# Optimization experiments

Hardware: AMD Instinct MI355X
Metric: run time of the kernel (lower is better)

The kernel has to match this reference:

```python
import jax, jax.numpy as jnp
import numpy as np

NL, B, L, D, V = 8, 8, 2048, 768, 50288
HALT_ID = 50277
EPS = 1e-5


def setup_inputs() -> dict:
    key = jax.random.key(0)
    ks = jax.random.split(key, 6)
    x_steps = jax.random.normal(ks[0], (NL, B, L, D), jnp.float32)
    residual_steps = jax.random.normal(ks[1], (NL, B, L, D), jnp.float32)
    norm_weight = jnp.ones((D,), jnp.float32)
    lm_head_weight = jax.random.normal(ks[2], (V, D), jnp.float32) * 0.02
    ans_starts = jax.random.randint(ks[3], (B,), 1, L)            # valid answer positions
    chain_lens = jax.random.randint(ks[4], (B,), 1, NL + 1)       # ragged chain lengths
    chain_targets = jax.random.randint(ks[5], (B, NL), 0, V)
    # last target of each chain is <HALT> (as in training data)
    chain_targets = chain_targets.at[jnp.arange(B), chain_lens - 1].set(HALT_ID)
    return {
        "x_steps": x_steps,
        "residual_steps": residual_steps,
        "norm_weight": norm_weight,
        "lm_head_weight": lm_head_weight,
        "ans_starts": ans_starts,
        "chain_targets": chain_targets,
        "chain_lens": chain_lens,
    }


def _forward(x_steps, residual_steps, norm_weight, lm_head_weight,
             ans_starts, chain_targets, chain_lens):
    n_loops, Bn, Ln, Dn = x_steps.shape
    Vn = lm_head_weight.shape[0]
    b_idx = jnp.arange(Bn)

    # gather the single answer position per batch (logits_step[b, as_-1, :])
    pos = jnp.clip(ans_starts - 1, 0, Ln - 1)                     # [B]
    xg = x_steps[:, b_idx, pos]                                   # [NL,B,D]
    rg = residual_steps[:, b_idx, pos]                            # [NL,B,D]

    # norm_f(x, residual, prenorm=False) == RMSNorm(x + residual)
    h = xg + rg
    h = h * jax.lax.rsqrt(jnp.mean(h * h, axis=-1, keepdims=True) + EPS) * norm_weight

    # lm_head on the gathered positions only (same math as full logits + gather)
    logits = jnp.einsum("lbd,vd->lbv", h, lm_head_weight)         # [NL,B,V]

    # target id: btgt[min(loop_i, len(btgt)-1)]
    loop_i = jnp.arange(n_loops)[:, None]                         # [NL,1]
    tidx = jnp.minimum(loop_i, chain_lens[None, :] - 1)           # [NL,B]
    tgt = chain_targets[b_idx[None, :], tidx]                     # [NL,B]

    valid = (ans_starts[None, :] >= 1) & (ans_starts[None, :] < Ln) & (tgt < Vn)
    vf = valid.astype(jnp.float32)

    # full-vocab cross entropy per (loop, batch)
    logZ = jax.scipy.special.logsumexp(logits, axis=-1)           # [NL,B]
    tgt_logit = jnp.take_along_axis(logits, tgt[..., None], axis=-1)[..., 0]
    ce = logZ - tgt_logit                                         # [NL,B]

    pred = jnp.argmax(logits, axis=-1)                            # [NL,B]
    correct = (pred == tgt).astype(jnp.float32)

    cnt = vf.sum(axis=1)                                          # valid per loop
    has = cnt > 0
    hasf = has.astype(jnp.float32)
    denom = jnp.maximum(cnt, 1.0)
    loop_loss = jnp.where(has, (ce * vf).sum(axis=1) / denom, 0.0)
    loop_acc = jnp.where(has, (correct * vf).sum(axis=1) / denom, 0.0)

    n_has = hasf.sum()
    avg_loss = (loop_loss * hasf).sum() / jnp.maximum(n_has, 1.0)
    avg_acc = (loop_acc * hasf).sum() / jnp.maximum(n_has, 1.0)

    # answer_acc = mean of step_accs[:-1] (drop last valid loop) if >1 valid loop
    last_valid = n_loops - 1 - jnp.argmax(has[::-1])
    drop_last = hasf * (jnp.arange(n_loops) != last_valid).astype(jnp.float32)
    ans_mask = jnp.where(n_has > 1, drop_last, hasf)
    answer_acc = jnp.where(ans_mask.sum() > 0,
                           (loop_acc * ans_mask).sum() / jnp.maximum(ans_mask.sum(), 1.0),
                           avg_acc)

    hm = vf * (tgt == HALT_ID).astype(jnp.float32)
    halt_acc = jnp.where(hm.sum() > 0,
                         (correct * hm).sum() / jnp.maximum(hm.sum(), 1.0),
                         0.0)
    return avg_loss, avg_acc, answer_acc, halt_acc


def reference(x_steps, residual_steps, norm_weight, lm_head_weight,
              ans_starts, chain_targets, chain_lens):
    return _forward(x_steps, residual_steps, norm_weight, lm_head_weight,
                    ans_starts, chain_targets, chain_lens)
```

## Files before the change

### kernel.cpp

```cpp
#include <hip/hip_runtime.h>
#include <hip/hip_bf16.h>
#include <math.h>

#define NLOOP 8
#define BB 8
#define LLEN 2048
#define DD 768
#define VV 50288
#define HALT 50277
#define EPSF 1e-5f

#define BN 64
#define BKK 32
#define KSTEPS (DD / BKK)
#define NBLK ((VV + BN - 1) / BN)
#define PFD 6

typedef short bf16x8 __attribute__((ext_vector_type(8)));
typedef float f32x4 __attribute__((ext_vector_type(4)));

#define LGKM_BARRIER() asm volatile("s_waitcnt lgkmcnt(0)\n\ts_barrier" ::: "memory")

__device__ __forceinline__ unsigned short f32_to_bf16(float f) {
    unsigned u = __builtin_bit_cast(unsigned, f);
    unsigned r = (u + 0x7FFFu + ((u >> 16) & 1u)) >> 16;
    return (unsigned short)r;
}

__global__ __launch_bounds__(256) void k_prep(
    const float* __restrict__ x, const float* __restrict__ res,
    const float* __restrict__ nw, const float* __restrict__ W,
    const int* __restrict__ ans_starts, const int* __restrict__ chain_targets,
    const int* __restrict__ chain_lens,
    unsigned short* __restrict__ hbf, float* __restrict__ tgt_logit,
    unsigned int* __restrict__ counter)
{
    if (blockIdx.x == 0 && threadIdx.x == 0) *counter = 0u;

    int lb = blockIdx.x, l = lb >> 3, b = lb & 7;
    int tid = threadIdx.x, lane = tid & 63, wave = tid >> 6;
    int as = ans_starts[b];
    int pos = as - 1;
    pos = pos < 0 ? 0 : (pos > LLEN - 1 ? LLEN - 1 : pos);
    size_t base = ((size_t)lb * LLEN + (size_t)pos) * DD;

    float hv[3];
    float ss = 0.f;
#pragma unroll
    for (int i = 0; i < 3; ++i) {
        int d = tid + i * 256;
        float v = x[base + d] + res[base + d];
        hv[i] = v;
        ss += v * v;
    }
#pragma unroll
    for (int off = 32; off; off >>= 1) ss += __shfl_down(ss, off);
    __shared__ float red[4];
    __shared__ float bc;
    if (lane == 0) red[wave] = ss;
    __syncthreads();
    if (tid == 0) bc = red[0] + red[1] + red[2] + red[3];
    __syncthreads();
    float rs = rsqrtf(bc / (float)DD + EPSF);

    int cl = chain_lens[b];
    int tix = l < cl - 1 ? l : cl - 1;
    int tgt = chain_targets[b * NLOOP + tix];
    bool tok = (tgt >= 0) && (tgt < VV);

    float dp = 0.f;
#pragma unroll
    for (int i = 0; i < 3; ++i) {
        int d = tid + i * 256;
        float h = hv[i] * rs * nw[d];
        hbf[(size_t)lb * DD + d] = f32_to_bf16(h);
        if (tok) dp += h * W[(size_t)tgt * DD + d];
    }
#pragma unroll
    for (int off = 32; off; off >>= 1) dp += __shfl_down(dp, off);
    __syncthreads();
    if (lane == 0) red[wave] = dp;
    __syncthreads();
    if (tid == 0) tgt_logit[lb] = red[0] + red[1] + red[2] + red[3];
}

__global__ __launch_bounds__(256, 2) void k_logits(
    const float* __restrict__ W, const unsigned short* __restrict__ hbf,
    float* __restrict__ pmax, float* __restrict__ psum, int* __restrict__ parg)
{
    __shared__ unsigned short Bs[2][64 * 56];

    int blk = blockIdx.x;
    int v0 = blk * BN;
    int tid = threadIdx.x;
    int wave = tid >> 6, lane = tid & 63, q = lane >> 4, c = lane & 15;

    const unsigned short* Ap = hbf + (size_t)(16 * wave + c) * DD + q * 8;
    bf16x8 A[KSTEPS];
#pragma unroll
    for (int ks = 0; ks < KSTEPS; ++ks)
        A[ks] = *(const bf16x8*)(Ap + ks * BKK);

    int r1 = tid >> 3, koff = (tid & 7) * 4;
    int vB0 = v0 + r1, vB1 = v0 + r1 + 32;
    const float* gB0 = W + (size_t)(vB0 < VV ? vB0 : 0) * DD + koff;
    const float* gB1 = W + (size_t)(vB1 < VV ? vB1 : 0) * DD + koff;

    f32x4 acc[4];
#pragma unroll
    for (int n = 0; n < 4; ++n) acc[n] = (f32x4){0.f, 0.f, 0.f, 0.f};

    auto stage_write = [&](int bufi, const f32x4& ra, const f32x4& rb) {
        ushort4 w0, w1;
        w0.x = f32_to_bf16(ra[0]); w0.y = f32_to_bf16(ra[1]);
        w0.z = f32_to_bf16(ra[2]); w0.w = f32_to_bf16(ra[3]);
        w1.x = f32_to_bf16(rb[0]); w1.y = f32_to_bf16(rb[1]);
        w1.z = f32_to_bf16(rb[2]); w1.w = f32_to_bf16(rb[3]);
        *(ushort4*)&Bs[bufi][r1 * 56 + koff] = w0;
        *(ushort4*)&Bs[bufi][(r1 + 32) * 56 + koff] = w1;
    };
    auto mfma_step = [&](int bufi, int ks) {
        bf16x8 f0 = *(const bf16x8*)&Bs[bufi][(c +  0) * 56 + q * 8];
        bf16x8 f1 = *(const bf16x8*)&Bs[bufi][(c + 16) * 56 + q * 8];
        bf16x8 f2 = *(const bf16x8*)&Bs[bufi][(c + 32) * 56 + q * 8];
        bf16x8 f3 = *(const bf16x8*)&Bs[bufi][(c + 48) * 56 + q * 8];
        acc[0] = __builtin_amdgcn_mfma_f32_16x16x32_bf16(A[ks], f0, acc[0], 0, 0, 0);
        acc[1] = __builtin_amdgcn_mfma_f32_16x16x32_bf16(A[ks], f1, acc[1], 0, 0, 0);
        acc[2] = __builtin_amdgcn_mfma_f32_16x16x32_bf16(A[ks], f2, acc[2], 0, 0, 0);
        acc[3] = __builtin_amdgcn_mfma_f32_16x16x32_bf16(A[ks], f3, acc[3], 0, 0, 0);
    };

    f32x4 pa[PFD], pb[PFD];
#pragma unroll
    for (int i = 0; i < PFD; ++i) {
        pa[i] = __builtin_nontemporal_load((const f32x4*)(gB0 + i * BKK));
        pb[i] = __builtin_nontemporal_load((const f32x4*)(gB1 + i * BKK));
    }

#pragma unroll
    for (int ks = 0; ks < KSTEPS; ++ks) {
        const int slot = ks % PFD;
        const int bufi = ks & 1;
        stage_write(bufi, pa[slot], pb[slot]);
        LGKM_BARRIER();
        if (ks + PFD < KSTEPS) {
            pa[slot] = __builtin_nontemporal_load((const f32x4*)(gB0 + (ks + PFD) * BKK));
            pb[slot] = __builtin_nontemporal_load((const f32x4*)(gB1 + (ks + PFD) * BKK));
        }
        mfma_step(bufi, ks);
    }

    const float NEGINF = -__builtin_inff();
#pragma unroll
    for (int r = 0; r < 4; ++r) {
        float val = NEGINF; int idx = 0x7fffffff;
#pragma unroll
        for (int n = 0; n < 4; ++n) {
            int colg = v0 + 16 * n + c;
            float v = (colg < VV) ? acc[n][r] : NEGINF;
            if (v > val || (v == val && colg < idx)) { val = v; idx = colg; }
        }
#pragma unroll
        for (int off = 1; off < 16; off <<= 1) {
            float ov = __shfl_xor(val, off);
            int oi = __shfl_xor(idx, off);
            if (ov > val || (ov == val && oi < idx)) { val = ov; idx = oi; }
        }
        float M = val;
        float e = 0.f;
#pragma unroll
        for (int n = 0; n < 4; ++n) {
            int colg = v0 + 16 * n + c;
            e += (colg < VV) ? __expf(acc[n][r] - M) : 0.f;
        }
#pragma unroll
        for (int off = 1; off < 16; off <<= 1) e += __shfl_xor(e, off);
        if (c == 0) {
            int row = 16 * wave + 4 * q + r;
            pmax[(size_t)row * NBLK + blk] = M;
            psum[(size_t)row * NBLK + blk] = e;
            parg[(size_t)row * NBLK + blk] = idx;
        }
    }
}

__global__ __launch_bounds__(256) void k_combine(
    const float* __restrict__ pmax, const float* __restrict__ psum,
    const int* __restrict__ parg, const float* __restrict__ tgt_logit,
    const int* __restrict__ ans_starts, const int* __restrict__ chain_targets,
    const int* __restrict__ chain_lens,
    float* __restrict__ logZ, int* __restrict__ pred,
    unsigned int* __restrict__ counter, float* __restrict__ out)
{
    int r = blockIdx.x;
    int tid = threadIdx.x;
    int wave = tid >> 6, lane = tid & 63;
    const float NEGINF = -__builtin_inff();

    const float* pm = pmax + (size_t)r * NBLK;
    const float* ps = psum + (size_t)r * NBLK;
    const int*   pa = parg + (size_t)r * NBLK;

    float M = NEGINF; int A_ = 0x7fffffff;
    for (int i = tid; i < NBLK; i += 256) {
        float m = pm[i];
        int a = pa[i];
        if (m > M || (m == M && a < A_)) { M = m; A_ = a; }
    }
#pragma unroll
    for (int off = 1; off < 64; off <<= 1) {
        float ov = __shfl_xor(M, off);
        int oa = __shfl_xor(A_, off);
        if (ov > M || (ov == M && oa < A_)) { M = ov; A_ = oa; }
    }
    __shared__ float sm[4]; __shared__ int sa[4]; __shared__ float ssum[4];
    __shared__ int lastflag;
    if (lane == 0) { sm[wave] = M; sa[wave] = A_; }
    __syncthreads();
    if (tid == 0) {
#pragma unroll
        for (int w = 1; w < 4; ++w)
            if (sm[w] > sm[0] || (sm[w] == sm[0] && sa[w] < sa[0])) { sm[0] = sm[w]; sa[0] = sa[w]; }
    }
    __syncthreads();
    float Mg = sm[0];

    float S = 0.f;
    for (int i = tid; i < NBLK; i += 256)
        S += ps[i] * __expf(pm[i] - Mg);
#pragma unroll
    for (int off = 1; off < 64; off <<= 1) S += __shfl_xor(S, off);
    if (lane == 0) ssum[wave] = S;
    __syncthreads();
    if (tid == 0) {
        float lz = Mg + logf(ssum[0] + ssum[1] + ssum[2] + ssum[3]);
        __hip_atomic_store(&logZ[r], lz, __ATOMIC_RELAXED, __HIP_MEMORY_SCOPE_AGENT);
        __hip_atomic_store(&pred[r], sa[0], __ATOMIC_RELAXED, __HIP_MEMORY_SCOPE_AGENT);
        __threadfence();
        unsigned int old = atomicAdd(counter, 1u);
        lastflag = (old == 63u) ? 1 : 0;
    }
    __syncthreads();
    if (lastflag == 0) return;

    __threadfence();
    __shared__ float lzs[64]; __shared__ int prs[64];
    if (tid < 64) {
        lzs[tid] = __hip_atomic_load(&logZ[tid], __ATOMIC_RELAXED, __HIP_MEMORY_SCOPE_AGENT);
        prs[tid] = __hip_atomic_load(&pred[tid], __ATOMIC_RELAXED, __HIP_MEMORY_SCOPE_AGENT);
    }
    __syncthreads();
    if (tid == 0) {
        float loop_loss[NLOOP], loop_acc[NLOOP], hasf[NLOOP];
        float n_has = 0.f, hms = 0.f, hcs = 0.f;
        for (int l = 0; l < NLOOP; ++l) {
            float cnt = 0.f, se = 0.f, sc = 0.f;
            for (int b = 0; b < BB; ++b) {
                int cl = chain_lens[b];
                int ti = l < cl - 1 ? l : cl - 1;
                int tgt = chain_targets[b * NLOOP + ti];
                int as = ans_starts[b];
                bool valid = (as >= 1) && (as < LLEN) && (tgt < VV);
                int idx = l * BB + b;
                float ce = lzs[idx] - tgt_logit[idx];
                float corr = (prs[idx] == tgt) ? 1.f : 0.f;
                if (valid) {
                    cnt += 1.f; se += ce; sc += corr;
                    if (tgt == HALT) { hms += 1.f; hcs += corr; }
                }
            }
            bool has = cnt > 0.f;
            hasf[l] = has ? 1.f : 0.f;
            n_has += hasf[l];
            float denom = cnt > 1.f ? cnt : 1.f;
            loop_loss[l] = has ? se / denom : 0.f;
            loop_acc[l]  = has ? sc / denom : 0.f;
        }
        float nn = n_has > 1.f ? n_has : 1.f;
        float avg_loss = 0.f, avg_acc = 0.f;
        for (int l = 0; l < NLOOP; ++l) {
            avg_loss += loop_loss[l] * hasf[l];
            avg_acc  += loop_acc[l]  * hasf[l];
        }
        avg_loss /= nn; avg_acc /= nn;
        int last_valid = NLOOP - 1;
        for (int l = NLOOP - 1; l >= 0; --l) if (hasf[l] > 0.f) { last_valid = l; break; }
        float ams = 0.f, aacc = 0.f;
        for (int l = 0; l < NLOOP; ++l) {
            float mask = (n_has > 1.f) ? (hasf[l] * ((l != last_valid) ? 1.f : 0.f)) : hasf[l];
            ams += mask; aacc += loop_acc[l] * mask;
        }
        float answer_acc = (ams > 0.f) ? (aacc / (ams > 1.f ? ams : 1.f)) : avg_acc;
        float halt_acc = (hms > 0.f) ? (hcs / (hms > 1.f ? hms : 1.f)) : 0.f;
        out[0] = avg_loss; out[1] = avg_acc; out[2] = answer_acc; out[3] = halt_acc;
    }
}

extern "C" void kernel_launch(void* const* d_in, const int* in_sizes, int n_in,
                              void* d_out, int out_size, void* d_ws, size_t ws_size,
                              hipStream_t stream) {
    const float* x   = (const float*)d_in[0];
    const float* res = (const float*)d_in[1];
    const float* nw  = (const float*)d_in[2];
    const float* W   = (const float*)d_in[3];
    const int* ans   = (const int*)d_in[4];
    const int* ct    = (const int*)d_in[5];
    const int* cl    = (const int*)d_in[6];
    float* out = (float*)d_out;

    char* ws = (char*)d_ws;
    unsigned short* hbf = (unsigned short*)ws;
    float* tgtl = (float*)(ws + 98304);
    size_t off = 98560;
    float* pmax = (float*)(ws + off);  off += (size_t)64 * NBLK * 4;
    float* psum = (float*)(ws + off);  off += (size_t)64 * NBLK * 4;
    int*   parg = (int*)  (ws + off);  off += (size_t)64 * NBLK * 4;
    float* logZ = (float*)(ws + off);  off += 256;
    int*   pred = (int*)  (ws + off);  off += 256;
    unsigned int* counter = (unsigned int*)(ws + off); off += 256;

    k_prep<<<64, 256, 0, stream>>>(x, res, nw, W, ans, ct, cl, hbf, tgtl, counter);
    k_logits<<<NBLK, 256, 0, stream>>>(W, hbf, pmax, psum, parg);
    k_combine<<<64, 256, 0, stream>>>(pmax, psum, parg, tgtl, ans, ct, cl,
                                      logZ, pred, counter, out);
}
```

Before: 59.82 us.

## Fuse prep, logits and combine into one persistent kernel with atomic grid sync

Merges the three kernels into one launch. The first 64 blocks compute the RMSNorm rows while every block prefetches its W tile, and all blocks spin on an atomic counter until the normalized rows are ready. The last 64 blocks to finish then do the per-row softmax combine, and the final block computes the metrics. The vocabulary tile grows from 64 to 128 rows with a shallower prefetch, and the non-temporal loads become plain loads. This removes launch gaps and lets the W stream start before the norm is done. It relies on all 393 blocks being co-resident, which the spin-waits need to avoid deadlock.

```diff
diff --git a/kernel.cpp b/kernel.cpp
--- a/kernel.cpp
+++ b/kernel.cpp
@@ -10,11 +10,11 @@
 #define HALT 50277
 #define EPSF 1e-5f
 
-#define BN 64
+#define BN2 128
 #define BKK 32
 #define KSTEPS (DD / BKK)
-#define NBLK ((VV + BN - 1) / BN)
-#define PFD 6
+#define NBLK2 ((VV + BN2 - 1) / BN2)
+#define PFD 4
 
 typedef short bf16x8 __attribute__((ext_vector_type(8)));
 typedef float f32x4 __attribute__((ext_vector_type(4)));
@@ -27,73 +27,96 @@
     return (unsigned short)r;
 }
 
-__global__ __launch_bounds__(256) void k_prep(
+__global__ __launch_bounds__(256, 2) void k_fused(
     const float* __restrict__ x, const float* __restrict__ res,
     const float* __restrict__ nw, const float* __restrict__ W,
     const int* __restrict__ ans_starts, const int* __restrict__ chain_targets,
     const int* __restrict__ chain_lens,
-    unsigned short* __restrict__ hbf, float* __restrict__ tgt_logit,
-    unsigned int* __restrict__ counter)
+    unsigned short* __restrict__ hbf, float* __restrict__ tgtl,
+    float* __restrict__ pmax, float* __restrict__ psum, int* __restrict__ parg,
+    float* __restrict__ logZ, int* __restrict__ pred,
+    unsigned int* __restrict__ counters, float* __restrict__ out)
 {
-    if (blockIdx.x == 0 && threadIdx.x == 0) *counter = 0u;
-
-    int lb = blockIdx.x, l = lb >> 3, b = lb & 7;
-    int tid = threadIdx.x, lane = tid & 63, wave = tid >> 6;
-    int as = ans_starts[b];
-    int pos = as - 1;
-    pos = pos < 0 ? 0 : (pos > LLEN - 1 ? LLEN - 1 : pos);
-    size_t base = ((size_t)lb * LLEN + (size_t)pos) * DD;
-
-    float hv[3];
-    float ss = 0.f;
-#pragma unroll
-    for (int i = 0; i < 3; ++i) {
-        int d = tid + i * 256;
-        float v = x[base + d] + res[base + d];
-        hv[i] = v;
-        ss += v * v;
-    }
-#pragma unroll
-    for (int off = 32; off; off >>= 1) ss += __shfl_down(ss, off);
-    __shared__ float red[4];
-    __shared__ float bc;
-    if (lane == 0) red[wave] = ss;
-    __syncthreads();
-    if (tid == 0) bc = red[0] + red[1] + red[2] + red[3];
-    __syncthreads();
-    float rs = rsqrtf(bc / (float)DD + EPSF);
-
-    int cl = chain_lens[b];
-    int tix = l < cl - 1 ? l : cl - 1;
-    int tgt = chain_targets[b * NLOOP + tix];
-    bool tok = (tgt >= 0) && (tgt < VV);
-
-    float dp = 0.f;
-#pragma unroll
-    for (int i = 0; i < 3; ++i) {
-        int d = tid + i * 256;
-        float h = hv[i] * rs * nw[d];
-        hbf[(size_t)lb * DD + d] = f32_to_bf16(h);
-        if (tok) dp += h * W[(size_t)tgt * DD + d];
-    }
-#pragma unroll
-    for (int off = 32; off; off >>= 1) dp += __shfl_down(dp, off);
-    __syncthreads();
-    if (lane == 0) red[wave] = dp;
-    __syncthreads();
-    if (tid == 0) tgt_logit[lb] = red[0] + red[1] + red[2] + red[3];
-}
-
-__global__ __launch_bounds__(256, 2) void k_logits(
-    const float* __restrict__ W, const unsigned short* __restrict__ hbf,
-    float* __restrict__ pmax, float* __restrict__ psum, int* __restrict__ parg)
-{
-    __shared__ unsigned short Bs[2][64 * 56];
-
-    int blk = blockIdx.x;
-    int v0 = blk * BN;
+    __shared__ unsigned short Bs[2][BN2 * 56];
+
+    int bid = blockIdx.x;
     int tid = threadIdx.x;
     int wave = tid >> 6, lane = tid & 63, q = lane >> 4, c = lane & 15;
+    int v0 = bid * BN2;
+
+    int r1 = tid >> 3, koff = (tid & 7) * 4;
+    int vB0 = v0 + r1, vB1 = v0 + r1 + 32, vB2 = v0 + r1 + 64, vB3 = v0 + r1 + 96;
+    const float* gB0 = W + (size_t)(vB0 < VV ? vB0 : 0) * DD + koff;
+    const float* gB1 = W + (size_t)(vB1 < VV ? vB1 : 0) * DD + koff;
+    const float* gB2 = W + (size_t)(vB2 < VV ? vB2 : 0) * DD + koff;
+    const float* gB3 = W + (size_t)(vB3 < VV ? vB3 : 0) * DD + koff;
+
+    f32x4 pf0[PFD], pf1[PFD], pf2[PFD], pf3[PFD];
+#pragma unroll
+    for (int i = 0; i < PFD; ++i) {
+        pf0[i] = *(const f32x4*)(gB0 + i * BKK);
+        pf1[i] = *(const f32x4*)(gB1 + i * BKK);
+        pf2[i] = *(const f32x4*)(gB2 + i * BKK);
+        pf3[i] = *(const f32x4*)(gB3 + i * BKK);
+    }
+
+    if (bid < 64) {
+        int b = bid & 7, l = bid >> 3;
+        int as = ans_starts[b];
+        int pos = as - 1;
+        pos = pos < 0 ? 0 : (pos > LLEN - 1 ? LLEN - 1 : pos);
+        size_t base = ((size_t)bid * LLEN + (size_t)pos) * DD;
+
+        float hv[3];
+        float ss = 0.f;
+#pragma unroll
+        for (int i = 0; i < 3; ++i) {
+            int d = tid + i * 256;
+            float v = x[base + d] + res[base + d];
+            hv[i] = v;
+            ss += v * v;
+        }
+#pragma unroll
+        for (int off = 32; off; off >>= 1) ss += __shfl_down(ss, off);
+        __shared__ float red[4];
+        __shared__ float bc;
+        if (lane == 0) red[wave] = ss;
+        __syncthreads();
+        if (tid == 0) bc = red[0] + red[1] + red[2] + red[3];
+        __syncthreads();
+        float rs = rsqrtf(bc / (float)DD + EPSF);
+
+        int cl = chain_lens[b];
+        int tix = l < cl - 1 ? l : cl - 1;
+        int tgt = chain_targets[b * NLOOP + tix];
+        bool tok = (tgt >= 0) && (tgt < VV);
+
+        float dp = 0.f;
+#pragma unroll
+        for (int i = 0; i < 3; ++i) {
+            int d = tid + i * 256;
+            float h = hv[i] * rs * nw[d];
+            hbf[(size_t)bid * DD + d] = f32_to_bf16(h);
+            if (tok) dp += h * W[(size_t)tgt * DD + d];
+        }
+#pragma unroll
+        for (int off = 32; off; off >>= 1) dp += __shfl_down(dp, off);
+        __syncthreads();
+        if (lane == 0) red[wave] = dp;
+        __syncthreads();
+        if (tid == 0) tgtl[bid] = red[0] + red[1] + red[2] + red[3];
+
+        __threadfence();
+        __syncthreads();
+        if (tid == 0) atomicAdd(&counters[0], 1u);
+    }
+
+    if (tid == 0) {
+        while (__hip_atomic_load(&counters[0], __ATOMIC_ACQUIRE, __HIP_MEMORY_SCOPE_AGENT) < 64u)
+            __builtin_amdgcn_s_sleep(8);
+    }
+    __syncthreads();
+    __threadfence();
 
     const unsigned short* Ap = hbf + (size_t)(16 * wave + c) * DD + q * 8;
     bf16x8 A[KSTEPS];
@@ -101,53 +124,37 @@
     for (int ks = 0; ks < KSTEPS; ++ks)
         A[ks] = *(const bf16x8*)(Ap + ks * BKK);
 
-    int r1 = tid >> 3, koff = (tid & 7) * 4;
-    int vB0 = v0 + r1, vB1 = v0 + r1 + 32;
-    const float* gB0 = W + (size_t)(vB0 < VV ? vB0 : 0) * DD + koff;
-    const float* gB1 = W + (size_t)(vB1 < VV ? vB1 : 0) * DD + koff;
-
-    f32x4 acc[4];
-#pragma unroll
-    for (int n = 0; n < 4; ++n) acc[n] = (f32x4){0.f, 0.f, 0.f, 0.f};
-
-    auto stage_write = [&](int bufi, const f32x4& ra, const f32x4& rb) {
-        ushort4 w0, w1;
-        w0.x = f32_to_bf16(ra[0]); w0.y = f32_to_bf16(ra[1]);
-        w0.z = f32_to_bf16(ra[2]); w0.w = f32_to_bf16(ra[3]);
-        w1.x = f32_to_bf16(rb[0]); w1.y = f32_to_bf16(rb[1]);
-        w1.z = f32_to_bf16(rb[2]); w1.w = f32_to_bf16(rb[3]);
-        *(ushort4*)&Bs[bufi][r1 * 56 + koff] = w0;
-        *(ushort4*)&Bs[bufi][(r1 + 32) * 56 + koff] = w1;
+    f32x4 acc[8];
+#pragma unroll
+    for (int n = 0; n < 8; ++n) acc[n] = (f32x4){0.f, 0.f, 0.f, 0.f};
+
+    auto st_row = [&](int bufi, int row, const f32x4& v) {
+        ushort4 w0;
+        w0.x = f32_to_bf16(v[0]); w0.y = f32_to_bf16(v[1]);
+        w0.z = f32_to_bf16(v[2]); w0.w = f32_to_bf16(v[3]);
+        *(ushort4*)&Bs[bufi][row * 56 + koff] = w0;
     };
-    auto mfma_step = [&](int bufi, int ks) {
-        bf16x8 f0 = *(const bf16x8*)&Bs[bufi][(c +  0) * 56 + q * 8];
-        bf16x8 f1 = *(const bf16x8*)&Bs[bufi][(c + 16) * 56 + q * 8];
-        bf16x8 f2 = *(const bf16x8*)&Bs[bufi][(c + 32) * 56 + q * 8];
-        bf16x8 f3 = *(const bf16x8*)&Bs[bufi][(c + 48) * 56 + q * 8];
-        acc[0] = __builtin_amdgcn_mfma_f32_16x16x32_bf16(A[ks], f0, acc[0], 0, 0, 0);
-        acc[1] = __builtin_amdgcn_mfma_f32_16x16x32_bf16(A[ks], f1, acc[1], 0, 0, 0);
-        acc[2] = __builtin_amdgcn_mfma_f32_16x16x32_bf16(A[ks], f2, acc[2], 0, 0, 0);
-        acc[3] = __builtin_amdgcn_mfma_f32_16x16x32_bf16(A[ks], f3, acc[3], 0, 0, 0);
-    };
-
-    f32x4 pa[PFD], pb[PFD];
-#pragma unroll
-    for (int i = 0; i < PFD; ++i) {
-        pa[i] = __builtin_nontemporal_load((const f32x4*)(gB0 + i * BKK));
-        pb[i] = __builtin_nontemporal_load((const f32x4*)(gB1 + i * BKK));
-    }
 
 #pragma unroll
     for (int ks = 0; ks < KSTEPS; ++ks) {
         const int slot = ks % PFD;
         const int bufi = ks & 1;
-        stage_write(bufi, pa[slot], pb[slot]);
+        st_row(bufi, r1,      pf0[slot]);
+        st_row(bufi, r1 + 32, pf1[slot]);
+        st_row(bufi, r1 + 64, pf2[slot]);
+        st_row(bufi, r1 + 96, pf3[slot]);
         LGKM_BARRIER();
         if (ks + PFD < KSTEPS) {
-            pa[slot] = __builtin_nontemporal_load((const f32x4*)(gB0 + (ks + PFD) * BKK));
-            pb[slot] = __builtin_nontemporal_load((const f32x4*)(gB1 + (ks + PFD) * BKK));
-        }
-        mfma_step(bufi, ks);
+            pf0[slot] = *(const f32x4*)(gB0 + (ks + PFD) * BKK);
+            pf1[slot] = *(const f32x4*)(gB1 + (ks + PFD) * BKK);
+            pf2[slot] = *(const f32x4*)(gB2 + (ks + PFD) * BKK);
+            pf3[slot] = *(const f32x4*)(gB3 + (ks + PFD) * BKK);
+        }
+#pragma unroll
+        for (int n = 0; n < 8; ++n) {
+            bf16x8 f = *(const bf16x8*)&Bs[bufi][(c + 16 * n) * 56 + q * 8];
+            acc[n] = __builtin_amdgcn_mfma_f32_16x16x32_bf16(A[ks], f, acc[n], 0, 0, 0);
+        }
     }
 
     const float NEGINF = -__builtin_inff();
@@ -155,7 +162,7 @@
     for (int r = 0; r < 4; ++r) {
         float val = NEGINF; int idx = 0x7fffffff;
 #pragma unroll
-        for (int n = 0; n < 4; ++n) {
+        for (int n = 0; n < 8; ++n) {
             int colg = v0 + 16 * n + c;
             float v = (colg < VV) ? acc[n][r] : NEGINF;
             if (v > val || (v == val && colg < idx)) { val = v; idx = colg; }
@@ -169,7 +176,7 @@
         float M = val;
         float e = 0.f;
 #pragma unroll
-        for (int n = 0; n < 4; ++n) {
+        for (int n = 0; n < 8; ++n) {
             int colg = v0 + 16 * n + c;
             e += (colg < VV) ? __expf(acc[n][r] - M) : 0.f;
         }
@@ -177,122 +184,125 @@
         for (int off = 1; off < 16; off <<= 1) e += __shfl_xor(e, off);
         if (c == 0) {
             int row = 16 * wave + 4 * q + r;
-            pmax[(size_t)row * NBLK + blk] = M;
-            psum[(size_t)row * NBLK + blk] = e;
-            parg[(size_t)row * NBLK + blk] = idx;
-        }
-    }
-}
-
-__global__ __launch_bounds__(256) void k_combine(
-    const float* __restrict__ pmax, const float* __restrict__ psum,
-    const int* __restrict__ parg, const float* __restrict__ tgt_logit,
-    const int* __restrict__ ans_starts, const int* __restrict__ chain_targets,
-    const int* __restrict__ chain_lens,
-    float* __restrict__ logZ, int* __restrict__ pred,
-    unsigned int* __restrict__ counter, float* __restrict__ out)
-{
-    int r = blockIdx.x;
-    int tid = threadIdx.x;
-    int wave = tid >> 6, lane = tid & 63;
-    const float NEGINF = -__builtin_inff();
-
-    const float* pm = pmax + (size_t)r * NBLK;
-    const float* ps = psum + (size_t)r * NBLK;
-    const int*   pa = parg + (size_t)r * NBLK;
-
-    float M = NEGINF; int A_ = 0x7fffffff;
-    for (int i = tid; i < NBLK; i += 256) {
-        float m = pm[i];
-        int a = pa[i];
-        if (m > M || (m == M && a < A_)) { M = m; A_ = a; }
-    }
-#pragma unroll
-    for (int off = 1; off < 64; off <<= 1) {
-        float ov = __shfl_xor(M, off);
-        int oa = __shfl_xor(A_, off);
-        if (ov > M || (ov == M && oa < A_)) { M = ov; A_ = oa; }
-    }
-    __shared__ float sm[4]; __shared__ int sa[4]; __shared__ float ssum[4];
-    __shared__ int lastflag;
-    if (lane == 0) { sm[wave] = M; sa[wave] = A_; }
+            pmax[(size_t)row * NBLK2 + bid] = M;
+            psum[(size_t)row * NBLK2 + bid] = e;
+            parg[(size_t)row * NBLK2 + bid] = idx;
+        }
+    }
+
+    __threadfence();
     __syncthreads();
+    __shared__ unsigned int s_old;
+    if (tid == 0) s_old = atomicAdd(&counters[1], 1u);
+    __syncthreads();
+    int crow = (int)s_old - (NBLK2 - 64);
+    if (crow < 0) return;
+
     if (tid == 0) {
-#pragma unroll
-        for (int w = 1; w < 4; ++w)
-            if (sm[w] > sm[0] || (sm[w] == sm[0] && sa[w] < sa[0])) { sm[0] = sm[w]; sa[0] = sa[w]; }
+        while (__hip_atomic_load(&counters[1], __ATOMIC_ACQUIRE, __HIP_MEMORY_SCOPE_AGENT) < (unsigned)NBLK2)
+            __builtin_amdgcn_s_sleep(8);
     }
     __syncthreads();
-    float Mg = sm[0];
-
-    float S = 0.f;
-    for (int i = tid; i < NBLK; i += 256)
-        S += ps[i] * __expf(pm[i] - Mg);
-#pragma unroll
-    for (int off = 1; off < 64; off <<= 1) S += __shfl_xor(S, off);
-    if (lane == 0) ssum[wave] = S;
-    __syncthreads();
-    if (tid == 0) {
-        float lz = Mg + logf(ssum[0] + ssum[1] + ssum[2] + ssum[3]);
-        __hip_atomic_store(&logZ[r], lz, __ATOMIC_RELAXED, __HIP_MEMORY_SCOPE_AGENT);
-        __hip_atomic_store(&pred[r], sa[0], __ATOMIC_RELAXED, __HIP_MEMORY_SCOPE_AGENT);
+    __threadfence();
+
+    {
+        const float* pm = pmax + (size_t)crow * NBLK2;
+        const float* ps = psum + (size_t)crow * NBLK2;
+        const int*   pa = parg + (size_t)crow * NBLK2;
+
+        float M = NEGINF; int A_ = 0x7fffffff;
+        for (int i = tid; i < NBLK2; i += 256) {
+            float m = pm[i];
+            int a = pa[i];
+            if (m > M || (m == M && a < A_)) { M = m; A_ = a; }
+        }
+#pragma unroll
+        for (int off = 1; off < 64; off <<= 1) {
+            float ov = __shfl_xor(M, off);
+            int oa = __shfl_xor(A_, off);
+            if (ov > M || (ov == M && oa < A_)) { M = ov; A_ = oa; }
+        }
+        __shared__ float sm[4]; __shared__ int sa[4]; __shared__ float ssum[4];
+        __shared__ int lastflag;
+        if (lane == 0) { sm[wave] = M; sa[wave] = A_; }
+        __syncthreads();
+        if (tid == 0) {
+#pragma unroll
+            for (int w = 1; w < 4; ++w)
+                if (sm[w] > sm[0] || (sm[w] == sm[0] && sa[w] < sa[0])) { sm[0] = sm[w]; sa[0] = sa[w]; }
+        }
+        __syncthreads();
+        float Mg = sm[0];
+
+        float S = 0.f;
+        for (int i = tid; i < NBLK2; i += 256)
+            S += ps[i] * __expf(pm[i] - Mg);
+#pragma unroll
+        for (int off = 1; off < 64; off <<= 1) S += __shfl_xor(S, off);
+        if (lane == 0) ssum[wave] = S;
+        __syncthreads();
+        if (tid == 0) {
+            float lz = Mg + logf(ssum[0] + ssum[1] + ssum[2] + ssum[3]);
+            __hip_atomic_store(&logZ[crow], lz, __ATOMIC_RELAXED, __HIP_MEMORY_SCOPE_AGENT);
+            __hip_atomic_store(&pred[crow], sa[0], __ATOMIC_RELAXED, __HIP_MEMORY_SCOPE_AGENT);
+            __threadfence();
+            unsigned int old2 = atomicAdd(&counters[2], 1u);
+            lastflag = (old2 == 63u) ? 1 : 0;
+        }
+        __syncthreads();
+        if (lastflag == 0) return;
+
         __threadfence();
-        unsigned int old = atomicAdd(counter, 1u);
-        lastflag = (old == 63u) ? 1 : 0;
-    }
-    __syncthreads();
-    if (lastflag == 0) return;
-
-    __threadfence();
-    __shared__ float lzs[64]; __shared__ int prs[64];
-    if (tid < 64) {
-        lzs[tid] = __hip_atomic_load(&logZ[tid], __ATOMIC_RELAXED, __HIP_MEMORY_SCOPE_AGENT);
-        prs[tid] = __hip_atomic_load(&pred[tid], __ATOMIC_RELAXED, __HIP_MEMORY_SCOPE_AGENT);
-    }
-    __syncthreads();
-    if (tid == 0) {
-        float loop_loss[NLOOP], loop_acc[NLOOP], hasf[NLOOP];
-        float n_has = 0.f, hms = 0.f, hcs = 0.f;
-        for (int l = 0; l < NLOOP; ++l) {
-            float cnt = 0.f, se = 0.f, sc = 0.f;
-            for (int b = 0; b < BB; ++b) {
-                int cl = chain_lens[b];
-                int ti = l < cl - 1 ? l : cl - 1;
-                int tgt = chain_targets[b * NLOOP + ti];
-                int as = ans_starts[b];
-                bool valid = (as >= 1) && (as < LLEN) && (tgt < VV);
-                int idx = l * BB + b;
-                float ce = lzs[idx] - tgt_logit[idx];
-                float corr = (prs[idx] == tgt) ? 1.f : 0.f;
-                if (valid) {
-                    cnt += 1.f; se += ce; sc += corr;
-                    if (tgt == HALT) { hms += 1.f; hcs += corr; }
+        __shared__ float lzs[64]; __shared__ int prs[64];
+        if (tid < 64) {
+            lzs[tid] = __hip_atomic_load(&logZ[tid], __ATOMIC_RELAXED, __HIP_MEMORY_SCOPE_AGENT);
+            prs[tid] = __hip_atomic_load(&pred[tid], __ATOMIC_RELAXED, __HIP_MEMORY_SCOPE_AGENT);
+        }
+        __syncthreads();
+        if (tid == 0) {
+            float loop_loss[NLOOP], loop_acc[NLOOP], hasf[NLOOP];
+            float n_has = 0.f, hms = 0.f, hcs = 0.f;
+            for (int l = 0; l < NLOOP; ++l) {
+                float cnt = 0.f, se = 0.f, sc = 0.f;
+                for (int b = 0; b < BB; ++b) {
+                    int cl = chain_lens[b];
+                    int ti = l < cl - 1 ? l : cl - 1;
+                    int tgt = chain_targets[b * NLOOP + ti];
+                    int as = ans_starts[b];
+                    bool valid = (as >= 1) && (as < LLEN) && (tgt < VV);
+                    int idx = l * BB + b;
+                    float ce = lzs[idx] - tgtl[idx];
+                    float corr = (prs[idx] == tgt) ? 1.f : 0.f;
+                    if (valid) {
+                        cnt += 1.f; se += ce; sc += corr;
+                        if (tgt == HALT) { hms += 1.f; hcs += corr; }
+                    }
                 }
+                bool has = cnt > 0.f;
+                hasf[l] = has ? 1.f : 0.f;
+                n_has += hasf[l];
+                float denom = cnt > 1.f ? cnt : 1.f;
+                loop_loss[l] = has ? se / denom : 0.f;
+                loop_acc[l]  = has ? sc / denom : 0.f;
             }
-            bool has = cnt > 0.f;
-            hasf[l] = has ? 1.f : 0.f;
-            n_has += hasf[l];
-            float denom = cnt > 1.f ? cnt : 1.f;
-            loop_loss[l] = has ? se / denom : 0.f;
-            loop_acc[l]  = has ? sc / denom : 0.f;
-        }
-        float nn = n_has > 1.f ? n_has : 1.f;
-        float avg_loss = 0.f, avg_acc = 0.f;
-        for (int l = 0; l < NLOOP; ++l) {
-            avg_loss += loop_loss[l] * hasf[l];
-            avg_acc  += loop_acc[l]  * hasf[l];
-        }
-        avg_loss /= nn; avg_acc /= nn;
-        int last_valid = NLOOP - 1;
-        for (int l = NLOOP - 1; l >= 0; --l) if (hasf[l] > 0.f) { last_valid = l; break; }
-        float ams = 0.f, aacc = 0.f;
-        for (int l = 0; l < NLOOP; ++l) {
-            float mask = (n_has > 1.f) ? (hasf[l] * ((l != last_valid) ? 1.f : 0.f)) : hasf[l];
-            ams += mask; aacc += loop_acc[l] * mask;
-        }
-        float answer_acc = (ams > 0.f) ? (aacc / (ams > 1.f ? ams : 1.f)) : avg_acc;
-        float halt_acc = (hms > 0.f) ? (hcs / (hms > 1.f ? hms : 1.f)) : 0.f;
-        out[0] = avg_loss; out[1] = avg_acc; out[2] = answer_acc; out[3] = halt_acc;
+            float nn = n_has > 1.f ? n_has : 1.f;
+            float avg_loss = 0.f, avg_acc = 0.f;
+            for (int l = 0; l < NLOOP; ++l) {
+                avg_loss += loop_loss[l] * hasf[l];
+                avg_acc  += loop_acc[l]  * hasf[l];
+            }
+            avg_loss /= nn; avg_acc /= nn;
+            int last_valid = NLOOP - 1;
+            for (int l = NLOOP - 1; l >= 0; --l) if (hasf[l] > 0.f) { last_valid = l; break; }
+            float ams = 0.f, aacc = 0.f;
+            for (int l = 0; l < NLOOP; ++l) {
+                float mask = (n_has > 1.f) ? (hasf[l] * ((l != last_valid) ? 1.f : 0.f)) : hasf[l];
+                ams += mask; aacc += loop_acc[l] * mask;
+            }
+            float answer_acc = (ams > 0.f) ? (aacc / (ams > 1.f ? ams : 1.f)) : avg_acc;
+            float halt_acc = (hms > 0.f) ? (hcs / (hms > 1.f ? hms : 1.f)) : 0.f;
+            out[0] = avg_loss; out[1] = avg_acc; out[2] = answer_acc; out[3] = halt_acc;
+        }
     }
 }
 
@@ -312,15 +322,15 @@
     unsigned short* hbf = (unsigned short*)ws;
     float* tgtl = (float*)(ws + 98304);
     size_t off = 98560;
-    float* pmax = (float*)(ws + off);  off += (size_t)64 * NBLK * 4;
-    float* psum = (float*)(ws + off);  off += (size_t)64 * NBLK * 4;
-    int*   parg = (int*)  (ws + off);  off += (size_t)64 * NBLK * 4;
+    float* pmax = (float*)(ws + off);  off += (size_t)64 * NBLK2 * 4;
+    float* psum = (float*)(ws + off);  off += (size_t)64 * NBLK2 * 4;
+    int*   parg = (int*)  (ws + off);  off += (size_t)64 * NBLK2 * 4;
     float* logZ = (float*)(ws + off);  off += 256;
     int*   pred = (int*)  (ws + off);  off += 256;
-    unsigned int* counter = (unsigned int*)(ws + off); off += 256;
-
-    k_prep<<<64, 256, 0, stream>>>(x, res, nw, W, ans, ct, cl, hbf, tgtl, counter);
-    k_logits<<<NBLK, 256, 0, stream>>>(W, hbf, pmax, psum, parg);
-    k_combine<<<64, 256, 0, stream>>>(pmax, psum, parg, tgtl, ans, ct, cl,
-                                      logZ, pred, counter, out);
+    unsigned int* counters = (unsigned int*)(ws + off); off += 256;
+
+    hipMemsetAsync(counters, 0, 16, stream);
+    k_fused<<<NBLK2, 256, 0, stream>>>(x, res, nw, W, ans, ct, cl,
+                                       hbf, tgtl, pmax, psum, parg,
+                                       logZ, pred, counters, out);
 }
```

New measurement: 169.2 us. 2.83x slower.

## Stage full-K quarter tiles of lm_head rows in swizzled LDS

Applied to the files above, without the earlier changes.

The logits kernel now splits each 64-row vocab block into four 16-row quarters. For each quarter it loads the full 768-wide fp32 rows in long contiguous per-thread chunks, converts them to bf16, and writes them into an XOR-swizzled, double-buffered LDS tile. Each quarter then runs all 24 MFMA k-steps at once, so the kernel needs 4 barriers instead of 24 and global reads are more contiguous. In exchange it uses much more LDS per block and more prefetch registers. It also drops the nontemporal load hints, which may affect occupancy and cache behaviour.

```diff
diff --git a/kernel.cpp b/kernel.cpp
--- a/kernel.cpp
+++ b/kernel.cpp
@@ -14,7 +14,7 @@
 #define BKK 32
 #define KSTEPS (DD / BKK)
 #define NBLK ((VV + BN - 1) / BN)
-#define PFD 6
+#define QROWS 16
 
 typedef short bf16x8 __attribute__((ext_vector_type(8)));
 typedef float f32x4 __attribute__((ext_vector_type(4)));
@@ -88,67 +88,68 @@
     const float* __restrict__ W, const unsigned short* __restrict__ hbf,
     float* __restrict__ pmax, float* __restrict__ psum, int* __restrict__ parg)
 {
-    __shared__ unsigned short Bs[2][64 * 56];
+    __shared__ unsigned short Qs[2][QROWS * 768];
 
     int blk = blockIdx.x;
     int v0 = blk * BN;
     int tid = threadIdx.x;
-    int wave = tid >> 6, lane = tid & 63, q = lane >> 4, c = lane & 15;
-
-    const unsigned short* Ap = hbf + (size_t)(16 * wave + c) * DD + q * 8;
+    int wave = tid >> 6, lane = tid & 63, qd = lane >> 4, c = lane & 15;
+
+    int rq = tid >> 4;
+    int p  = tid & 15;
+
+    f32x4 pfA[12], pfB[12];
+
+    auto issueq = [&](f32x4* pf, int q) {
+        int gr = v0 + q * QROWS + rq;
+        if (gr >= VV) gr = 0;
+        const float* src = W + (size_t)gr * DD + p * 48;
+#pragma unroll
+        for (int i = 0; i < 12; ++i) pf[i] = *(const f32x4*)(src + i * 4);
+    };
+    auto stageq = [&](const f32x4* pf, int buf) {
+#pragma unroll
+        for (int j = 0; j < 6; ++j) {
+            bf16x8 v;
+            v[0] = (short)f32_to_bf16(pf[2 * j][0]);
+            v[1] = (short)f32_to_bf16(pf[2 * j][1]);
+            v[2] = (short)f32_to_bf16(pf[2 * j][2]);
+            v[3] = (short)f32_to_bf16(pf[2 * j][3]);
+            v[4] = (short)f32_to_bf16(pf[2 * j + 1][0]);
+            v[5] = (short)f32_to_bf16(pf[2 * j + 1][1]);
+            v[6] = (short)f32_to_bf16(pf[2 * j + 1][2]);
+            v[7] = (short)f32_to_bf16(pf[2 * j + 1][3]);
+            int us = (p * 6 + j) ^ (rq & 7);
+            *(bf16x8*)&Qs[buf][rq * 768 + us * 8] = v;
+        }
+    };
+
+    issueq(pfA, 0);
+    issueq(pfB, 1);
+
+    const unsigned short* Ap = hbf + (size_t)(16 * wave + c) * DD + qd * 8;
     bf16x8 A[KSTEPS];
 #pragma unroll
     for (int ks = 0; ks < KSTEPS; ++ks)
         A[ks] = *(const bf16x8*)(Ap + ks * BKK);
 
-    int r1 = tid >> 3, koff = (tid & 7) * 4;
-    int vB0 = v0 + r1, vB1 = v0 + r1 + 32;
-    const float* gB0 = W + (size_t)(vB0 < VV ? vB0 : 0) * DD + koff;
-    const float* gB1 = W + (size_t)(vB1 < VV ? vB1 : 0) * DD + koff;
-
     f32x4 acc[4];
 #pragma unroll
     for (int n = 0; n < 4; ++n) acc[n] = (f32x4){0.f, 0.f, 0.f, 0.f};
 
-    auto stage_write = [&](int bufi, const f32x4& ra, const f32x4& rb) {
-        ushort4 w0, w1;
-        w0.x = f32_to_bf16(ra[0]); w0.y = f32_to_bf16(ra[1]);
-        w0.z = f32_to_bf16(ra[2]); w0.w = f32_to_bf16(ra[3]);
-        w1.x = f32_to_bf16(rb[0]); w1.y = f32_to_bf16(rb[1]);
-        w1.z = f32_to_bf16(rb[2]); w1.w = f32_to_bf16(rb[3]);
-        *(ushort4*)&Bs[bufi][r1 * 56 + koff] = w0;
-        *(ushort4*)&Bs[bufi][(r1 + 32) * 56 + koff] = w1;
+    auto mfmaq = [&](int buf, int q) {
+#pragma unroll
+        for (int ks = 0; ks < KSTEPS; ++ks) {
+            int us = (ks * 4 + qd) ^ (c & 7);
+            bf16x8 f = *(const bf16x8*)&Qs[buf][c * 768 + us * 8];
+            acc[q] = __builtin_amdgcn_mfma_f32_16x16x32_bf16(A[ks], f, acc[q], 0, 0, 0);
+        }
     };
-    auto mfma_step = [&](int bufi, int ks) {
-        bf16x8 f0 = *(const bf16x8*)&Bs[bufi][(c +  0) * 56 + q * 8];
-        bf16x8 f1 = *(const bf16x8*)&Bs[bufi][(c + 16) * 56 + q * 8];
-        bf16x8 f2 = *(const bf16x8*)&Bs[bufi][(c + 32) * 56 + q * 8];
-        bf16x8 f3 = *(const bf16x8*)&Bs[bufi][(c + 48) * 56 + q * 8];
-        acc[0] = __builtin_amdgcn_mfma_f32_16x16x32_bf16(A[ks], f0, acc[0], 0, 0, 0);
-        acc[1] = __builtin_amdgcn_mfma_f32_16x16x32_bf16(A[ks], f1, acc[1], 0, 0, 0);
-        acc[2] = __builtin_amdgcn_mfma_f32_16x16x32_bf16(A[ks], f2, acc[2], 0, 0, 0);
-        acc[3] = __builtin_amdgcn_mfma_f32_16x16x32_bf16(A[ks], f3, acc[3], 0, 0, 0);
-    };
-
-    f32x4 pa[PFD], pb[PFD];
-#pragma unroll
-    for (int i = 0; i < PFD; ++i) {
-        pa[i] = __builtin_nontemporal_load((const f32x4*)(gB0 + i * BKK));
-        pb[i] = __builtin_nontemporal_load((const f32x4*)(gB1 + i * BKK));
-    }
-
-#pragma unroll
-    for (int ks = 0; ks < KSTEPS; ++ks) {
-        const int slot = ks % PFD;
-        const int bufi = ks & 1;
-        stage_write(bufi, pa[slot], pb[slot]);
-        LGKM_BARRIER();
-        if (ks + PFD < KSTEPS) {
-            pa[slot] = __builtin_nontemporal_load((const f32x4*)(gB0 + (ks + PFD) * BKK));
-            pb[slot] = __builtin_nontemporal_load((const f32x4*)(gB1 + (ks + PFD) * BKK));
-        }
-        mfma_step(bufi, ks);
-    }
+
+    stageq(pfA, 0); LGKM_BARRIER(); issueq(pfA, 2); mfmaq(0, 0);
+    stageq(pfB, 1); LGKM_BARRIER(); issueq(pfB, 3); mfmaq(1, 1);
+    stageq(pfA, 0); LGKM_BARRIER();                 mfmaq(0, 2);
+    stageq(pfB, 1); LGKM_BARRIER();                 mfmaq(1, 3);
 
     const float NEGINF = -__builtin_inff();
 #pragma unroll
@@ -176,7 +177,7 @@
 #pragma unroll
         for (int off = 1; off < 16; off <<= 1) e += __shfl_xor(e, off);
         if (c == 0) {
-            int row = 16 * wave + 4 * q + r;
+            int row = 16 * wave + 4 * qd + r;
             pmax[(size_t)row * NBLK + blk] = M;
             psum[(size_t)row * NBLK + blk] = e;
             parg[(size_t)row * NBLK + blk] = idx;
```

After: 64.59 us. 8.0% more time.

## Fuse RMSNorm prep into logits kernel and take target logit from GEMM tile

Applied to the files above, without the earlier changes.

Removes the separate prep kernel. Each logits block now gathers x+residual at the answer position, computes the RMSNorm itself and builds its bf16 A fragments directly, so one launch and the round trip through global memory disappear. The target logit is taken from the MFMA accumulators of the block that owns the target column, instead of a separate fp32 dot product. The change also swizzles the LDS layout for the B tile without padding, uses 8-wide stores, and lowers the prefetch depth from 6 to 4 with plain loads. In exchange, every one of the ~786 blocks re-reads the 64 gathered rows (redundant but L2-resident), the target logit now carries bf16 rounding, and the norm is rounded twice.

```diff
diff --git a/kernel.cpp b/kernel.cpp
--- a/kernel.cpp
+++ b/kernel.cpp
@@ -14,7 +14,7 @@
 #define BKK 32
 #define KSTEPS (DD / BKK)
 #define NBLK ((VV + BN - 1) / BN)
-#define PFD 6
+#define PFD 4
 
 typedef short bf16x8 __attribute__((ext_vector_type(8)));
 typedef float f32x4 __attribute__((ext_vector_type(4)));
@@ -26,116 +26,107 @@
     unsigned r = (u + 0x7FFFu + ((u >> 16) & 1u)) >> 16;
     return (unsigned short)r;
 }
-
-__global__ __launch_bounds__(256) void k_prep(
+__device__ __forceinline__ float bf16_to_f32(unsigned short s) {
+    unsigned u = ((unsigned)s) << 16;
+    return __builtin_bit_cast(float, u);
+}
+
+__global__ __launch_bounds__(256, 2) void k_logits(
     const float* __restrict__ x, const float* __restrict__ res,
     const float* __restrict__ nw, const float* __restrict__ W,
     const int* __restrict__ ans_starts, const int* __restrict__ chain_targets,
     const int* __restrict__ chain_lens,
-    unsigned short* __restrict__ hbf, float* __restrict__ tgt_logit,
+    float* __restrict__ tgtl,
+    float* __restrict__ pmax, float* __restrict__ psum, int* __restrict__ parg,
     unsigned int* __restrict__ counter)
 {
-    if (blockIdx.x == 0 && threadIdx.x == 0) *counter = 0u;
-
-    int lb = blockIdx.x, l = lb >> 3, b = lb & 7;
-    int tid = threadIdx.x, lane = tid & 63, wave = tid >> 6;
-    int as = ans_starts[b];
-    int pos = as - 1;
-    pos = pos < 0 ? 0 : (pos > LLEN - 1 ? LLEN - 1 : pos);
-    size_t base = ((size_t)lb * LLEN + (size_t)pos) * DD;
-
-    float hv[3];
-    float ss = 0.f;
-#pragma unroll
-    for (int i = 0; i < 3; ++i) {
-        int d = tid + i * 256;
-        float v = x[base + d] + res[base + d];
-        hv[i] = v;
-        ss += v * v;
-    }
-#pragma unroll
-    for (int off = 32; off; off >>= 1) ss += __shfl_down(ss, off);
-    __shared__ float red[4];
-    __shared__ float bc;
-    if (lane == 0) red[wave] = ss;
-    __syncthreads();
-    if (tid == 0) bc = red[0] + red[1] + red[2] + red[3];
-    __syncthreads();
-    float rs = rsqrtf(bc / (float)DD + EPSF);
-
-    int cl = chain_lens[b];
-    int tix = l < cl - 1 ? l : cl - 1;
-    int tgt = chain_targets[b * NLOOP + tix];
-    bool tok = (tgt >= 0) && (tgt < VV);
-
-    float dp = 0.f;
-#pragma unroll
-    for (int i = 0; i < 3; ++i) {
-        int d = tid + i * 256;
-        float h = hv[i] * rs * nw[d];
-        hbf[(size_t)lb * DD + d] = f32_to_bf16(h);
-        if (tok) dp += h * W[(size_t)tgt * DD + d];
-    }
-#pragma unroll
-    for (int off = 32; off; off >>= 1) dp += __shfl_down(dp, off);
-    __syncthreads();
-    if (lane == 0) red[wave] = dp;
-    __syncthreads();
-    if (tid == 0) tgt_logit[lb] = red[0] + red[1] + red[2] + red[3];
-}
-
-__global__ __launch_bounds__(256, 2) void k_logits(
-    const float* __restrict__ W, const unsigned short* __restrict__ hbf,
-    float* __restrict__ pmax, float* __restrict__ psum, int* __restrict__ parg)
-{
-    __shared__ unsigned short Bs[2][64 * 56];
+    __shared__ unsigned short Bs[2][64 * 32];
 
     int blk = blockIdx.x;
     int v0 = blk * BN;
     int tid = threadIdx.x;
     int wave = tid >> 6, lane = tid & 63, q = lane >> 4, c = lane & 15;
 
-    const unsigned short* Ap = hbf + (size_t)(16 * wave + c) * DD + q * 8;
+    if (blk == 0 && tid == 0) *counter = 0u;
+
+    int r1 = tid >> 2, j2 = tid & 3;
+    int vB = v0 + r1;
+    const float* gB = W + (size_t)(vB < VV ? vB : 0) * DD + j2 * 8;
+
+    f32x4 pa[PFD], pb[PFD];
+#pragma unroll
+    for (int i = 0; i < PFD; ++i) {
+        pa[i] = *(const f32x4*)(gB + i * BKK);
+        pb[i] = *(const f32x4*)(gB + i * BKK + 4);
+    }
+
+    int rowa = 16 * wave + c;
+    int ba = rowa & 7;
+    int asb = ans_starts[ba];
+    int pos = asb - 1;
+    pos = pos < 0 ? 0 : (pos > LLEN - 1 ? LLEN - 1 : pos);
+    size_t abase = ((size_t)rowa * LLEN + (size_t)pos) * DD + q * 8;
+    const float* xp = x + abase;
+    const float* rp = res + abase;
+    const float* npw = nw + q * 8;
+
     bf16x8 A[KSTEPS];
-#pragma unroll
-    for (int ks = 0; ks < KSTEPS; ++ks)
-        A[ks] = *(const bf16x8*)(Ap + ks * BKK);
-
-    int r1 = tid >> 3, koff = (tid & 7) * 4;
-    int vB0 = v0 + r1, vB1 = v0 + r1 + 32;
-    const float* gB0 = W + (size_t)(vB0 < VV ? vB0 : 0) * DD + koff;
-    const float* gB1 = W + (size_t)(vB1 < VV ? vB1 : 0) * DD + koff;
+    float ss = 0.f;
+#pragma unroll
+    for (int j = 0; j < KSTEPS; ++j) {
+        f32x4 x0 = *(const f32x4*)(xp + j * BKK);
+        f32x4 x1 = *(const f32x4*)(xp + j * BKK + 4);
+        f32x4 r0 = *(const f32x4*)(rp + j * BKK);
+        f32x4 r1v = *(const f32x4*)(rp + j * BKK + 4);
+#pragma unroll
+        for (int e = 0; e < 4; ++e) {
+            float v = x0[e] + r0[e];
+            ss += v * v;
+            A[j][e] = (short)f32_to_bf16(v);
+            float w = x1[e] + r1v[e];
+            ss += w * w;
+            A[j][e + 4] = (short)f32_to_bf16(w);
+        }
+    }
+    ss += __shfl_xor(ss, 16);
+    ss += __shfl_xor(ss, 32);
+    float rs = rsqrtf(ss / (float)DD + EPSF);
+#pragma unroll
+    for (int j = 0; j < KSTEPS; ++j) {
+        f32x4 n0 = *(const f32x4*)(npw + j * BKK);
+        f32x4 n1 = *(const f32x4*)(npw + j * BKK + 4);
+#pragma unroll
+        for (int e = 0; e < 4; ++e) {
+            A[j][e]     = (short)f32_to_bf16(bf16_to_f32((unsigned short)A[j][e])     * rs * n0[e]);
+            A[j][e + 4] = (short)f32_to_bf16(bf16_to_f32((unsigned short)A[j][e + 4]) * rs * n1[e]);
+        }
+    }
 
     f32x4 acc[4];
 #pragma unroll
     for (int n = 0; n < 4; ++n) acc[n] = (f32x4){0.f, 0.f, 0.f, 0.f};
 
+    const int uw = (j2 ^ ((r1 >> 1) & 3)) * 8;
+    const int ur = (q ^ ((c >> 1) & 3)) * 8;
+
     auto stage_write = [&](int bufi, const f32x4& ra, const f32x4& rb) {
-        ushort4 w0, w1;
-        w0.x = f32_to_bf16(ra[0]); w0.y = f32_to_bf16(ra[1]);
-        w0.z = f32_to_bf16(ra[2]); w0.w = f32_to_bf16(ra[3]);
-        w1.x = f32_to_bf16(rb[0]); w1.y = f32_to_bf16(rb[1]);
-        w1.z = f32_to_bf16(rb[2]); w1.w = f32_to_bf16(rb[3]);
-        *(ushort4*)&Bs[bufi][r1 * 56 + koff] = w0;
-        *(ushort4*)&Bs[bufi][(r1 + 32) * 56 + koff] = w1;
+        bf16x8 v;
+        v[0] = (short)f32_to_bf16(ra[0]); v[1] = (short)f32_to_bf16(ra[1]);
+        v[2] = (short)f32_to_bf16(ra[2]); v[3] = (short)f32_to_bf16(ra[3]);
+        v[4] = (short)f32_to_bf16(rb[0]); v[5] = (short)f32_to_bf16(rb[1]);
+        v[6] = (short)f32_to_bf16(rb[2]); v[7] = (short)f32_to_bf16(rb[3]);
+        *(bf16x8*)&Bs[bufi][r1 * 32 + uw] = v;
     };
     auto mfma_step = [&](int bufi, int ks) {
-        bf16x8 f0 = *(const bf16x8*)&Bs[bufi][(c +  0) * 56 + q * 8];
-        bf16x8 f1 = *(const bf16x8*)&Bs[bufi][(c + 16) * 56 + q * 8];
-        bf16x8 f2 = *(const bf16x8*)&Bs[bufi][(c + 32) * 56 + q * 8];
-        bf16x8 f3 = *(const bf16x8*)&Bs[bufi][(c + 48) * 56 + q * 8];
+        bf16x8 f0 = *(const bf16x8*)&Bs[bufi][(c +  0) * 32 + ur];
+        bf16x8 f1 = *(const bf16x8*)&Bs[bufi][(c + 16) * 32 + ur];
+        bf16x8 f2 = *(const bf16x8*)&Bs[bufi][(c + 32) * 32 + ur];
+        bf16x8 f3 = *(const bf16x8*)&Bs[bufi][(c + 48) * 32 + ur];
         acc[0] = __builtin_amdgcn_mfma_f32_16x16x32_bf16(A[ks], f0, acc[0], 0, 0, 0);
         acc[1] = __builtin_amdgcn_mfma_f32_16x16x32_bf16(A[ks], f1, acc[1], 0, 0, 0);
         acc[2] = __builtin_amdgcn_mfma_f32_16x16x32_bf16(A[ks], f2, acc[2], 0, 0, 0);
         acc[3] = __builtin_amdgcn_mfma_f32_16x16x32_bf16(A[ks], f3, acc[3], 0, 0, 0);
     };
-
-    f32x4 pa[PFD], pb[PFD];
-#pragma unroll
-    for (int i = 0; i < PFD; ++i) {
-        pa[i] = __builtin_nontemporal_load((const f32x4*)(gB0 + i * BKK));
-        pb[i] = __builtin_nontemporal_load((const f32x4*)(gB1 + i * BKK));
-    }
 
 #pragma unroll
     for (int ks = 0; ks < KSTEPS; ++ks) {
@@ -144,8 +135,8 @@
         stage_write(bufi, pa[slot], pb[slot]);
         LGKM_BARRIER();
         if (ks + PFD < KSTEPS) {
-            pa[slot] = __builtin_nontemporal_load((const f32x4*)(gB0 + (ks + PFD) * BKK));
-            pb[slot] = __builtin_nontemporal_load((const f32x4*)(gB1 + (ks + PFD) * BKK));
+            pa[slot] = *(const f32x4*)(gB + (ks + PFD) * BKK);
+            pb[slot] = *(const f32x4*)(gB + (ks + PFD) * BKK + 4);
         }
         mfma_step(bufi, ks);
     }
@@ -180,6 +171,21 @@
             pmax[(size_t)row * NBLK + blk] = M;
             psum[(size_t)row * NBLK + blk] = e;
             parg[(size_t)row * NBLK + blk] = idx;
+        }
+    }
+
+#pragma unroll
+    for (int r = 0; r < 4; ++r) {
+        int row = 16 * wave + 4 * q + r;
+        int bb = row & 7, ll = row >> 3;
+        int cl_ = chain_lens[bb];
+        int tix = ll < cl_ - 1 ? ll : cl_ - 1;
+        int t = chain_targets[bb * NLOOP + tix];
+        int tr = t - v0;
+        if (tr >= 0 && tr < BN && (t & 15) == c) {
+#pragma unroll
+            for (int n = 0; n < 4; ++n)
+                if ((tr >> 4) == n) tgtl[row] = acc[n][r];
         }
     }
 }
@@ -309,9 +315,8 @@
     float* out = (float*)d_out;
 
     char* ws = (char*)d_ws;
-    unsigned short* hbf = (unsigned short*)ws;
-    float* tgtl = (float*)(ws + 98304);
-    size_t off = 98560;
+    float* tgtl = (float*)ws;
+    size_t off = 256;
     float* pmax = (float*)(ws + off);  off += (size_t)64 * NBLK * 4;
     float* psum = (float*)(ws + off);  off += (size_t)64 * NBLK * 4;
     int*   parg = (int*)  (ws + off);  off += (size_t)64 * NBLK * 4;
@@ -319,8 +324,8 @@
     int*   pred = (int*)  (ws + off);  off += 256;
     unsigned int* counter = (unsigned int*)(ws + off); off += 256;
 
-    k_prep<<<64, 256, 0, stream>>>(x, res, nw, W, ans, ct, cl, hbf, tgtl, counter);
-    k_logits<<<NBLK, 256, 0, stream>>>(W, hbf, pmax, psum, parg);
+    k_logits<<<NBLK, 256, 0, stream>>>(x, res, nw, W, ans, ct, cl,
+                                       tgtl, pmax, psum, parg, counter);
     k_combine<<<64, 256, 0, stream>>>(pmax, psum, parg, tgtl, ans, ct, cl,
                                       logZ, pred, counter, out);
 }
```

After: 102.8 us. 71.8% more time.
